# Optimization experiments

Hardware: AMD Instinct MI355X
Metric: run time of the kernel (lower is better)

## Reference

```python
import jax, jax.numpy as jnp
import numpy as np

N_NODES = 50000
N_EDGES = 800000
G_DIM = 128
H1 = 32
HEADS = 4
H2 = 64
ATT_SLOPE = 0.2   # PyG GATConv default negative_slope
LRELU_SLOPE = 0.01  # F.leaky_relu default
BN_EPS = 1e-5


def segment_softmax(logits, seg, num_segments):
    # numerically stable softmax over edges grouped by destination node
    m = jax.ops.segment_max(logits, seg, num_segments=num_segments)
    e = jnp.exp(logits - m[seg])
    s = jax.ops.segment_sum(e, seg, num_segments=num_segments)
    return e / (s[seg] + 1e-16)


def gat_layer(x, src, dst, W, a_src, a_dst, bias, concat):
    # PyG GATConv: x' = W x ; alpha_e = softmax_dst(leaky_relu(a_src.x_src + a_dst.x_dst))
    N = x.shape[0]
    H, C = a_src.shape
    xw = (x @ W).reshape(N, H, C)          # [N,H,C]
    al_s = jnp.sum(xw * a_src, axis=-1)    # [N,H]
    al_d = jnp.sum(xw * a_dst, axis=-1)    # [N,H]
    logits = jax.nn.leaky_relu(al_s[src] + al_d[dst], ATT_SLOPE)  # [E,H]
    alpha = segment_softmax(logits, dst, N)                        # [E,H]
    out = jax.ops.segment_sum(alpha[:, :, None] * xw[src], dst, num_segments=N)  # [N,H,C]
    out = out.reshape(N, H * C) if concat else out.mean(axis=1)
    return out + bias


def batchnorm_train(x, gamma, beta):
    mu = x.mean(axis=0)
    var = x.var(axis=0)  # biased, as torch BN uses for normalization
    return (x - mu) * jax.lax.rsqrt(var + BN_EPS) * gamma + beta


def setup_inputs() -> dict:
    key = jax.random.key(0)
    ks = jax.random.split(key, 12)
    node_features = jax.random.normal(ks[0], (N_NODES, G_DIM), dtype=jnp.float32)
    node_type = jax.random.randint(ks[1], (N_NODES,), 0, 3)
    edge_index = jax.random.randint(ks[2], (2, N_EDGES), 0, N_NODES)
    s1 = 1.0 / np.sqrt(G_DIM)
    s2 = 1.0 / np.sqrt(H1 * HEADS)
    return {
        "node_features": node_features,
        "node_type": node_type,
        "edge_index": edge_index,
        "W1": jax.random.normal(ks[3], (G_DIM, HEADS * H1), dtype=jnp.float32) * s1,
        "a_src1": jax.random.normal(ks[4], (HEADS, H1), dtype=jnp.float32) * s1,
        "a_dst1": jax.random.normal(ks[5], (HEADS, H1), dtype=jnp.float32) * s1,
        "b1": jnp.zeros((HEADS * H1,), dtype=jnp.float32),
        "g1": jnp.ones((HEADS * H1,), dtype=jnp.float32),
        "beta1": jnp.zeros((HEADS * H1,), dtype=jnp.float32),
        "W2": jax.random.normal(ks[6], (HEADS * H1, H2), dtype=jnp.float32) * s2,
        "a_src2": jax.random.normal(ks[7], (1, H2), dtype=jnp.float32) * s2,
        "a_dst2": jax.random.normal(ks[8], (1, H2), dtype=jnp.float32) * s2,
        "b2": jnp.zeros((H2,), dtype=jnp.float32),
        "g2": jnp.ones((H2,), dtype=jnp.float32),
        "beta2": jnp.zeros((H2,), dtype=jnp.float32),
    }


def reference(node_features, node_type, edge_index, W1, a_src1, a_dst1, b1, g1, beta1,
              W2, a_src2, a_dst2, b2, g2, beta2):
    N = node_features.shape[0]
    loop = jnp.arange(N)
    src = jnp.concatenate([edge_index[0], loop])  # add_self_loops=True (PyG default)
    dst = jnp.concatenate([edge_index[1], loop])
    x = gat_layer(node_features, src, dst, W1, a_src1, a_dst1, b1, concat=True)
    x = jax.nn.leaky_relu(batchnorm_train(x, g1, beta1), LRELU_SLOPE)
    x = gat_layer(x, src, dst, W2, a_src2, a_dst2, b2, concat=False)
    x = jax.nn.leaky_relu(batchnorm_train(x, g2, beta2), LRELU_SLOPE)
    return x
```

## Files before the change

kernel.cpp:

```cpp
#include <hip/hip_runtime.h>
#include <hip/hip_fp16.h>

#define NN 50000
#define NE 800000
#define ET 850000
#define GD 128
#define D1 128
#define NH 4
#define D2 64
#define NB_SCAN 196
#define NBP 1024
#define NXCD 8
#define NPX 6250
#define HSL 128
#define ESL 6250
#define NHB 1024
#define CAP 1024

typedef unsigned short u16;
typedef _Float16 half8_t __attribute__((ext_vector_type(8)));
typedef float    f32x4_t __attribute__((ext_vector_type(4)));

__device__ __forceinline__ float lrelu(float x, float s) { return x > 0.f ? x : s * x; }

__global__ void k_prepw(const float* __restrict__ W1, const float* __restrict__ W2,
                        __half* __restrict__ Wp1, __half* __restrict__ Wp2) {
    int idx = blockIdx.x * 256 + threadIdx.x;
    if (idx < 16384) {
        int i = idx & 7, l = (idx >> 3) & 63, nt = (idx >> 9) & 7, kk = idx >> 12;
        int k = kk * 32 + (l >> 4) * 8 + i, n = nt * 16 + (l & 15);
        Wp1[idx] = __float2half(W1[k * D1 + n]);
    } else if (idx < 24576) {
        int x2 = idx - 16384;
        int i = x2 & 7, l = (x2 >> 3) & 63, nt = (x2 >> 9) & 3, kk = x2 >> 11;
        int k = kk * 32 + (l >> 4) * 8 + i, n = nt * 16 + (l & 15);
        Wp2[x2] = __float2half(W2[k * D2 + n]);
    }
}

__global__ void k_histgemm1(const int* __restrict__ ei,
                            unsigned* __restrict__ ulist, u16* __restrict__ plist,
                            u16* __restrict__ partial, int* __restrict__ mcount,
                            const float* __restrict__ x, const half8_t* __restrict__ wp,
                            const float* __restrict__ as, const float* __restrict__ ad,
                            __half* __restrict__ xw, float* __restrict__ al_s,
                            float* __restrict__ al_d) {
    __shared__ unsigned lh[NPX / 2];
    __shared__ unsigned lk;
    if (blockIdx.x < NHB) {
        const int s = blockIdx.x & (NXCD - 1), j = blockIdx.x >> 3;
        const int lo = s * NPX;
        for (int i = threadIdx.x; i < NPX / 2; i += 256) lh[i] = 0u;
        if (threadIdx.x == 0) lk = 0u;
        __syncthreads();
        const int e0 = j * ESL;
        const size_t ub = (size_t)blockIdx.x * CAP;
        for (int e = e0 + threadIdx.x; e < e0 + ESL; e += 256) {
            int d = ei[NE + e];
            unsigned dl = (unsigned)(d - lo);
            if (dl < (unsigned)NPX) {
                unsigned old = atomicAdd(&lh[dl >> 1], (dl & 1) ? 0x10000u : 1u);
                unsigned p = (old >> ((dl & 1) * 16)) & 0xffffu;
                unsigned k = atomicAdd(&lk, 1u);
                if (k < CAP) {
                    ulist[ub + k] = (dl << 16) | (unsigned)ei[e];
                    plist[ub + k] = (u16)p;
                }
            }
        }
        __syncthreads();
        unsigned* pout = (unsigned*)(partial + (size_t)blockIdx.x * NPX);
        for (int i = threadIdx.x; i < NPX / 2; i += 256) pout[i] = lh[i];
        if (threadIdx.x == 0) mcount[blockIdx.x] = (int)lk;
        return;
    }
    const int strip = (blockIdx.x - NHB) * 4 + (threadIdx.x >> 6);
    if (strip >= NN / 16) return;
    const int l = threadIdx.x & 63;
    const int row0 = strip * 16;
    const int c = l & 15, g = l >> 4;
    const float* xrow = x + (size_t)(row0 + c) * GD;

    f32x4_t acc[8];
#pragma unroll
    for (int nt = 0; nt < 8; nt++) acc[nt] = (f32x4_t){0.f, 0.f, 0.f, 0.f};

#pragma unroll
    for (int kk = 0; kk < 4; kk++) {
        const int koff = kk * 32 + g * 8;
        f32x4_t a0 = *(const f32x4_t*)(xrow + koff);
        f32x4_t a1 = *(const f32x4_t*)(xrow + koff + 4);
        half8_t af;
#pragma unroll
        for (int i = 0; i < 4; i++) { af[i] = (_Float16)a0[i]; af[i + 4] = (_Float16)a1[i]; }
#pragma unroll
        for (int nt = 0; nt < 8; nt++) {
            half8_t bf = wp[(kk * 8 + nt) * 64 + l];
            acc[nt] = __builtin_amdgcn_mfma_f32_16x16x32_f16(af, bf, acc[nt], 0, 0, 0);
        }
    }

    float asv[8], adv[8];
#pragma unroll
    for (int nt = 0; nt < 8; nt++) { asv[nt] = as[nt * 16 + c]; adv[nt] = ad[nt * 16 + c]; }

#pragma unroll
    for (int r = 0; r < 4; r++) {
        const int row = row0 + g * 4 + r;
        __half* xwr = xw + (size_t)row * D1;
        float hs[4] = {0.f, 0.f, 0.f, 0.f}, hd[4] = {0.f, 0.f, 0.f, 0.f};
#pragma unroll
        for (int nt = 0; nt < 8; nt++) {
            float v = acc[nt][r];
            xwr[nt * 16 + c] = __float2half(v);
            hs[nt >> 1] += v * asv[nt];
            hd[nt >> 1] += v * adv[nt];
        }
#pragma unroll
        for (int m = 1; m <= 8; m <<= 1) {
#pragma unroll
            for (int h = 0; h < 4; h++) { hs[h] += __shfl_xor(hs[h], m); hd[h] += __shfl_xor(hd[h], m); }
        }
        if (c == 0) {
#pragma unroll
            for (int h = 0; h < 4; h++) { al_s[row * NH + h] = hs[h]; al_d[row * NH + h] = hd[h]; }
        }
    }
}

__global__ void k_nodeprefix(u16* __restrict__ partial, int* __restrict__ cnt) {
    int d = blockIdx.x * 256 + threadIdx.x;
    if (d >= NN) return;
    int s = d / NPX, dl = d - s * NPX;
    int run = 0;
    for (int j = 0; j < HSL; j++) {
        size_t idx = (size_t)(j * NXCD + s) * NPX + dl;
        int v = partial[idx];
        partial[idx] = (u16)run;
        run += v;
    }
    cnt[d] = run + 1;
}

__global__ void k_blocksum(const int* __restrict__ cnt, int* __restrict__ part) {
    __shared__ int r[256];
    int t = threadIdx.x, i = blockIdx.x * 256 + t;
    r[t] = (i < NN) ? cnt[i] : 0;
    __syncthreads();
    for (int s = 128; s >= 1; s >>= 1) {
        if (t < s) r[t] += r[t + s];
        __syncthreads();
    }
    if (t == 0) part[blockIdx.x] = r[0];
}

__global__ void k_scanfix(const int* __restrict__ cnt, const int* __restrict__ part,
                          int* __restrict__ row_ptr) {
    __shared__ int pp[256];
    __shared__ int r[256];
    int b = blockIdx.x, t = threadIdx.x, i = b * 256 + t;
    pp[t] = (t < NB_SCAN) ? part[t] : 0;
    int v = (i < NN) ? cnt[i] : 0;
    r[t] = v;
    __syncthreads();
    for (int off = 1; off < 256; off <<= 1) {
        int pv = (t >= off) ? pp[t - off] : 0;
        int rv = (t >= off) ? r[t - off] : 0;
        __syncthreads();
        pp[t] += pv; r[t] += rv;
        __syncthreads();
    }
    int pbase = b ? pp[b - 1] : 0;
    if (i < NN) row_ptr[i] = pbase + (t ? r[t - 1] : 0);
    if (i == NN - 1) row_ptr[NN] = pbase + r[t];
}

__global__ void k_fill_x(const int* __restrict__ row_ptr, const u16* __restrict__ P,
                         const unsigned* __restrict__ ulist, const u16* __restrict__ plist,
                         const int* __restrict__ mcount, u16* __restrict__ csr_src) {
    const int b = blockIdx.x;
    if (b < NHB) {
        const int s = b & (NXCD - 1);
        const int lo = s * NPX;
        const int m = min(mcount[b], CAP);
        const size_t ub = (size_t)b * CAP;
        const u16* Pb = P + (size_t)b * NPX;
        for (int k = threadIdx.x; k < m; k += 256) {
            unsigned u = ulist[ub + k];
            int dl = (int)(u >> 16);
            int base = row_ptr[lo + dl] + 1 + (int)Pb[dl] + (int)plist[ub + k];
            csr_src[base] = (u16)(u & 0xffffu);
        }
        return;
    }
    const int b2 = b - NHB;
    const int xcd = b2 & (NXCD - 1);
    const int off = (b2 >> 3) * 256 + threadIdx.x;
    if (off < NPX) {
        int d = xcd * NPX + off;
        csr_src[row_ptr[d]] = (u16)d;
    }
}

__global__ void k_gat1(const int* __restrict__ row_ptr, const u16* __restrict__ csr_src,
                       const float* __restrict__ als, const float* __restrict__ ald,
                       const __half2* __restrict__ xw, __half2* __restrict__ out) {
    const int b = blockIdx.x;
    const int d = (b & (NXCD - 1)) * NPX + (b >> 3);
    const int beg = row_ptr[d];
    const int deg = row_ptr[d + 1] - beg;
    const int lane = threadIdx.x;

    __shared__ int   s_src[64];
    __shared__ float s_al[64 * NH];

    const float4 adv = *(const float4*)(ald + d * NH);
    const int h = lane >> 4;

    float ax = 0.f, ay = 0.f, den = 0.f;
    for (int base = 0; base < deg; base += 64) {
        int cnt = min(64, deg - base);
        if (lane < cnt) {
            int s = csr_src[beg + base + lane];
            s_src[lane] = s;
            const float4 a = *(const float4*)(als + s * NH);
            s_al[lane * NH + 0] = __expf(lrelu(a.x + adv.x, 0.2f));
            s_al[lane * NH + 1] = __expf(lrelu(a.y + adv.y, 0.2f));
            s_al[lane * NH + 2] = __expf(lrelu(a.z + adv.z, 0.2f));
            s_al[lane * NH + 3] = __expf(lrelu(a.w + adv.w, 0.2f));
        }
        __syncthreads();
#pragma unroll 4
        for (int i = 0; i < cnt; i++) {
            float al = s_al[i * NH + h];
            float2 v = __half22float2(xw[(size_t)s_src[i] * 64 + lane]);
            den += al; ax += al * v.x; ay += al * v.y;
        }
        __syncthreads();
    }
    float inv = 1.f / (den + 1e-16f);
    __half2 hv;
    hv.x = __float2half(ax * inv);
    hv.y = __float2half(ay * inv);
    out[(size_t)d * 64 + lane] = hv;
}

__global__ void k_bnstats1h(const __half2* __restrict__ x, float* __restrict__ bp) {
    int t = threadIdx.x, bid = blockIdx.x;
    float s0 = 0.f, q0 = 0.f, s1 = 0.f, q1 = 0.f;
    for (int r = bid; r < NN; r += NBP) {
        float2 f = __half22float2(x[(size_t)r * 64 + t]);
        s0 += f.x; q0 += f.x * f.x;
        s1 += f.y; q1 += f.y * f.y;
    }
    bp[bid * D1 + 2 * t] = s0;
    bp[bid * D1 + 2 * t + 1] = s1;
    bp[NBP * D1 + bid * D1 + 2 * t] = q0;
    bp[NBP * D1 + bid * D1 + 2 * t + 1] = q1;
}

template <int D>
__global__ void k_bnstats(const float* __restrict__ x, float* __restrict__ bp) {
    int j = threadIdx.x, bid = blockIdx.x;
    float s = 0.f, q = 0.f;
    for (int r = bid; r < NN; r += NBP) {
        float v = x[(size_t)r * D + j];
        s += v; q += v * v;
    }
    bp[bid * D + j] = s;
    bp[NBP * D + bid * D + j] = q;
}

template <int D>
__global__ void k_bnreduce(const float* __restrict__ bp, const float* __restrict__ g,
                           const float* __restrict__ b, float* __restrict__ scale,
                           float* __restrict__ shift) {
    __shared__ float rs[256], rq[256];
    int j = blockIdx.x, t = threadIdx.x;
    float s = 0.f, q = 0.f;
    for (int i = t; i < NBP; i += 256) {
        s += bp[i * D + j];
        q += bp[NBP * D + i * D + j];
    }
    rs[t] = s; rq[t] = q;
    __syncthreads();
    for (int st = 128; st >= 1; st >>= 1) {
        if (t < st) { rs[t] += rs[t + st]; rq[t] += rq[t + st]; }
        __syncthreads();
    }
    if (t == 0) {
        float mu = rs[0] / (float)NN;
        float var = rq[0] / (float)NN - mu * mu;
        float sc = rsqrtf(var + 1e-5f) * g[j];
        scale[j] = sc;
        shift[j] = b[j] - mu * sc;
    }
}

__global__ void k_bnapply2(const float* __restrict__ x, const float* __restrict__ scale,
                           const float* __restrict__ shift, float* __restrict__ y) {
    int idx = blockIdx.x * blockDim.x + threadIdx.x;
    if (idx >= NN * D2 / 4) return;
    float4 v = ((const float4*)x)[idx];
    int c = (idx * 4) & (D2 - 1);
    v.x = lrelu(v.x * scale[c + 0] + shift[c + 0], 0.01f);
    v.y = lrelu(v.y * scale[c + 1] + shift[c + 1], 0.01f);
    v.z = lrelu(v.z * scale[c + 2] + shift[c + 2], 0.01f);
    v.w = lrelu(v.w * scale[c + 3] + shift[c + 3], 0.01f);
    ((float4*)y)[idx] = v;
}

__global__ void k_gemm2m(const __half* __restrict__ x, const float* __restrict__ scale,
                         const float* __restrict__ shift, const half8_t* __restrict__ wp,
                         const float* __restrict__ as, const float* __restrict__ ad,
                         __half* __restrict__ xw, float* __restrict__ al_s, float* __restrict__ al_d) {
    const int l = threadIdx.x;
    const int row0 = blockIdx.x * 16;
    const int c = l & 15, g = l >> 4;
    const __half* xrow = x + (size_t)(row0 + c) * D1;

    f32x4_t acc[4];
#pragma unroll
    for (int nt = 0; nt < 4; nt++) acc[nt] = (f32x4_t){0.f, 0.f, 0.f, 0.f};

#pragma unroll
    for (int kk = 0; kk < 4; kk++) {
        const int koff = kk * 32 + g * 8;
        half8_t a8 = *(const half8_t*)(xrow + koff);
        f32x4_t sc0 = *(const f32x4_t*)(scale + koff);
        f32x4_t sc1 = *(const f32x4_t*)(scale + koff + 4);
        f32x4_t sh0 = *(const f32x4_t*)(shift + koff);
        f32x4_t sh1 = *(const f32x4_t*)(shift + koff + 4);
        half8_t af;
#pragma unroll
        for (int i = 0; i < 4; i++) {
            af[i]     = (_Float16)lrelu((float)a8[i] * sc0[i] + sh0[i], 0.01f);
            af[i + 4] = (_Float16)lrelu((float)a8[i + 4] * sc1[i] + sh1[i], 0.01f);
        }
#pragma unroll
        for (int nt = 0; nt < 4; nt++) {
            half8_t bf = wp[(kk * 4 + nt) * 64 + l];
            acc[nt] = __builtin_amdgcn_mfma_f32_16x16x32_f16(af, bf, acc[nt], 0, 0, 0);
        }
    }

    float asv[4], adv[4];
#pragma unroll
    for (int nt = 0; nt < 4; nt++) { asv[nt] = as[nt * 16 + c]; adv[nt] = ad[nt * 16 + c]; }

#pragma unroll
    for (int r = 0; r < 4; r++) {
        const int row = row0 + g * 4 + r;
        __half* xwr = xw + (size_t)row * D2;
        float hs = 0.f, hd = 0.f;
#pragma unroll
        for (int nt = 0; nt < 4; nt++) {
            float v = acc[nt][r];
            xwr[nt * 16 + c] = __float2half(v);
            hs += v * asv[nt];
            hd += v * adv[nt];
        }
#pragma unroll
        for (int m = 1; m <= 8; m <<= 1) { hs += __shfl_xor(hs, m); hd += __shfl_xor(hd, m); }
        if (c == 0) { al_s[row] = hs; al_d[row] = hd; }
    }
}

__global__ void k_gat2(const int* __restrict__ row_ptr, const u16* __restrict__ csr_src,
                       const float* __restrict__ als, const float* __restrict__ ald,
                       const __half2* __restrict__ xw, float* __restrict__ out) {
    const int b = blockIdx.x;
    const int d = (b & (NXCD - 1)) * NPX + (b >> 3);
    const int beg = row_ptr[d];
    const int deg = row_ptr[d + 1] - beg;
    const int lane = threadIdx.x;
    const int sub = lane >> 5, l = lane & 31;

    const float add = ald[d];
    float ax = 0.f, ay = 0.f, den = 0.f;
    for (int base = 0; base < deg; base += 64) {
        int cnt = min(64, deg - base);
        int s = 0; float e = 0.f;
        if (lane < cnt) {
            s = csr_src[beg + base + lane];
            e = __expf(lrelu(als[s] + add, 0.2f));
        }
        int np = (cnt + 1) >> 1;
        for (int i = 0; i < np; i++) {
            int idx = 2 * i + sub;
            float al = __shfl(e, idx);
            int  si  = __shfl(s, idx);
            float2 v = __half22float2(xw[(size_t)si * 32 + l]);
            den += al; ax += al * v.x; ay += al * v.y;
        }
    }
    ax += __shfl_xor(ax, 32); ay += __shfl_xor(ay, 32); den += __shfl_xor(den, 32);
    if (lane < 32) {
        float inv = 1.f / (den + 1e-16f);
        *(float2*)(out + (size_t)d * D2 + 2 * l) = make_float2(ax * inv, ay * inv);
    }
}

extern "C" void kernel_launch(void* const* d_in, const int* in_sizes, int n_in,
                              void* d_out, int out_size, void* d_ws, size_t ws_size,
                              hipStream_t stream) {
    const float* x   = (const float*)d_in[0];
    const int*   ei  = (const int*)d_in[2];
    const float* W1  = (const float*)d_in[3];
    const float* as1 = (const float*)d_in[4];
    const float* ad1 = (const float*)d_in[5];
    const float* g1  = (const float*)d_in[7];
    const float* be1 = (const float*)d_in[8];
    const float* W2  = (const float*)d_in[9];
    const float* as2 = (const float*)d_in[10];
    const float* ad2 = (const float*)d_in[11];
    const float* g2  = (const float*)d_in[13];
    const float* be2 = (const float*)d_in[14];
    float* out = (float*)d_out;

    float* ws = (float*)d_ws;
    __half* xw1  = (__half*)ws;
    __half* xw2  = (__half*)ws;
    float* bp    = ws + 1600000;
    unsigned* ulist = (unsigned*)(ws + 3200000);
    u16*   plist  = (u16*)(ws + 4248576);
    int*   mcount = (int*)(ws + 4772864);
    int*   cnt    = (int*)(ws + 4773888);
    float* al_s2 = ws + 3200000;
    float* al_d2 = ws + 3250000;
    float* al_s1 = ws + 6400000;
    float* al_d1 = al_s1 + 200000;
    float* aggF  = al_d1 + 200000;
    __half* agg1 = (__half*)aggF;
    u16*   partial = (u16*)aggF;
    int*   row_ptr = (int*)(aggF + 3200000);
    int*   part    = row_ptr + 50001;
    float* st      = (float*)(part + 249);
    u16*   csr_src = (u16*)(st + 768);
    __half* Wp1    = (__half*)(csr_src + 850000);
    __half* Wp2    = Wp1 + 16384;

    k_prepw<<<96, 256, 0, stream>>>(W1, W2, Wp1, Wp2);
    k_histgemm1<<<NHB + (NN / 16 + 3) / 4, 256, 0, stream>>>(
        ei, ulist, plist, partial, mcount, x, (const half8_t*)Wp1, as1, ad1, xw1, al_s1, al_d1);
    k_nodeprefix<<<NB_SCAN, 256, 0, stream>>>(partial, cnt);
    k_blocksum<<<NB_SCAN, 256, 0, stream>>>(cnt, part);
    k_scanfix<<<NB_SCAN, 256, 0, stream>>>(cnt, part, row_ptr);
    k_fill_x<<<NHB + 200, 256, 0, stream>>>(row_ptr, partial, ulist, plist, mcount, csr_src);

    k_gat1<<<NN, 64, 0, stream>>>(row_ptr, csr_src, al_s1, al_d1, (const __half2*)xw1,
                                  (__half2*)agg1);
    k_bnstats1h<<<NBP, 64, 0, stream>>>((const __half2*)agg1, bp);
    k_bnreduce<D1><<<D1, 256, 0, stream>>>(bp, g1, be1, st, st + 128);

    k_gemm2m<<<NN / 16, 64, 0, stream>>>(agg1, st, st + 128, (const half8_t*)Wp2, as2, ad2,
                                         xw2, al_s2, al_d2);
    k_gat2<<<NN, 64, 0, stream>>>(row_ptr, csr_src, al_s2, al_d2, (const __half2*)xw2, out);
    k_bnstats<D2><<<NBP, D2, 0, stream>>>(out, bp);
    k_bnreduce<D2><<<D2, 256, 0, stream>>>(bp, g2, be2, st + 256, st + 320);
    k_bnapply2<<<(NN * D2 / 4 + 255) / 256, 256, 0, stream>>>(out, st + 256, st + 320, out);
}
```

Baseline: 182.2 us.

## Pack four destination nodes per block in GAT kernels and fuse prefix with blocksum

The two GAT aggregation kernels now handle four destination nodes per 256-thread block, one wavefront each, instead of one 64-thread block per node. This cuts block count and launch/scheduling overhead. k_gat1 also drops its shared-memory staging and __syncthreads, passing source indices and attention weights between lanes with shuffles. The per-node prefix kernel and the block-sum kernel are merged into one launch. The trade-off is five shuffles per edge in k_gat1 and some idle waves in the tail blocks.

After: 213.2 us. +17.0%, slower.

```diff
diff --git a/kernel.cpp b/kernel.cpp
--- a/kernel.cpp
+++ b/kernel.cpp
@@ -16,6 +16,7 @@
 #define ESL 6250
 #define NHB 1024
 #define CAP 1024
+#define NGB (NXCD * 1563)
 
 typedef unsigned short u16;
 typedef _Float16 half8_t __attribute__((ext_vector_type(8)));
@@ -128,27 +129,26 @@
     }
 }
 
-__global__ void k_nodeprefix(u16* __restrict__ partial, int* __restrict__ cnt) {
-    int d = blockIdx.x * 256 + threadIdx.x;
-    if (d >= NN) return;
-    int s = d / NPX, dl = d - s * NPX;
+__global__ void k_prefsum(u16* __restrict__ partial, int* __restrict__ cnt,
+                          int* __restrict__ part) {
+    __shared__ int r[256];
+    int t = threadIdx.x, d = blockIdx.x * 256 + t;
     int run = 0;
-    for (int j = 0; j < HSL; j++) {
-        size_t idx = (size_t)(j * NXCD + s) * NPX + dl;
-        int v = partial[idx];
-        partial[idx] = (u16)run;
-        run += v;
-    }
-    cnt[d] = run + 1;
-}
-
-__global__ void k_blocksum(const int* __restrict__ cnt, int* __restrict__ part) {
-    __shared__ int r[256];
-    int t = threadIdx.x, i = blockIdx.x * 256 + t;
-    r[t] = (i < NN) ? cnt[i] : 0;
+    if (d < NN) {
+        int s = d / NPX, dl = d - s * NPX;
+        for (int j = 0; j < HSL; j++) {
+            size_t idx = (size_t)(j * NXCD + s) * NPX + dl;
+            int v = partial[idx];
+            partial[idx] = (u16)run;
+            run += v;
+        }
+        run += 1;
+        cnt[d] = run;
+    }
+    r[t] = (d < NN) ? run : 0;
     __syncthreads();
-    for (int s = 128; s >= 1; s >>= 1) {
-        if (t < s) r[t] += r[t + s];
+    for (int s2 = 128; s2 >= 1; s2 >>= 1) {
+        if (t < s2) r[t] += r[t + s2];
         __syncthreads();
     }
     if (t == 0) part[blockIdx.x] = r[0];
@@ -205,38 +205,39 @@
 __global__ void k_gat1(const int* __restrict__ row_ptr, const u16* __restrict__ csr_src,
                        const float* __restrict__ als, const float* __restrict__ ald,
                        const __half2* __restrict__ xw, __half2* __restrict__ out) {
-    const int b = blockIdx.x;
-    const int d = (b & (NXCD - 1)) * NPX + (b >> 3);
+    const int bi = blockIdx.x;
+    const int s = bi & (NXCD - 1);
+    const int off = (bi >> 3) * 4 + (threadIdx.x >> 6);
+    if (off >= NPX) return;
+    const int d = s * NPX + off;
+    const int lane = threadIdx.x & 63;
     const int beg = row_ptr[d];
     const int deg = row_ptr[d + 1] - beg;
-    const int lane = threadIdx.x;
-
-    __shared__ int   s_src[64];
-    __shared__ float s_al[64 * NH];
+    const int h = lane >> 4;
 
     const float4 adv = *(const float4*)(ald + d * NH);
-    const int h = lane >> 4;
 
     float ax = 0.f, ay = 0.f, den = 0.f;
     for (int base = 0; base < deg; base += 64) {
         int cnt = min(64, deg - base);
+        int sv = 0;
+        float e0 = 0.f, e1 = 0.f, e2 = 0.f, e3 = 0.f;
         if (lane < cnt) {
-            int s = csr_src[beg + base + lane];
-            s_src[lane] = s;
-            const float4 a = *(const float4*)(als + s * NH);
-            s_al[lane * NH + 0] = __expf(lrelu(a.x + adv.x, 0.2f));
-            s_al[lane * NH + 1] = __expf(lrelu(a.y + adv.y, 0.2f));
-            s_al[lane * NH + 2] = __expf(lrelu(a.z + adv.z, 0.2f));
-            s_al[lane * NH + 3] = __expf(lrelu(a.w + adv.w, 0.2f));
-        }
-        __syncthreads();
-#pragma unroll 4
+            sv = csr_src[beg + base + lane];
+            const float4 a = *(const float4*)(als + sv * NH);
+            e0 = __expf(lrelu(a.x + adv.x, 0.2f));
+            e1 = __expf(lrelu(a.y + adv.y, 0.2f));
+            e2 = __expf(lrelu(a.z + adv.z, 0.2f));
+            e3 = __expf(lrelu(a.w + adv.w, 0.2f));
+        }
         for (int i = 0; i < cnt; i++) {
-            float al = s_al[i * NH + h];
-            float2 v = __half22float2(xw[(size_t)s_src[i] * 64 + lane]);
+            float a0 = __shfl(e0, i), a1 = __shfl(e1, i);
+            float a2 = __shfl(e2, i), a3 = __shfl(e3, i);
+            int   si = __shfl(sv, i);
+            float al = (h == 0) ? a0 : (h == 1) ? a1 : (h == 2) ? a2 : a3;
+            float2 v = __half22float2(xw[(size_t)si * 64 + lane]);
             den += al; ax += al * v.x; ay += al * v.y;
         }
-        __syncthreads();
     }
     float inv = 1.f / (den + 1e-16f);
     __half2 hv;
@@ -369,27 +370,30 @@
 __global__ void k_gat2(const int* __restrict__ row_ptr, const u16* __restrict__ csr_src,
                        const float* __restrict__ als, const float* __restrict__ ald,
                        const __half2* __restrict__ xw, float* __restrict__ out) {
-    const int b = blockIdx.x;
-    const int d = (b & (NXCD - 1)) * NPX + (b >> 3);
+    const int bi = blockIdx.x;
+    const int s = bi & (NXCD - 1);
+    const int off = (bi >> 3) * 4 + (threadIdx.x >> 6);
+    if (off >= NPX) return;
+    const int d = s * NPX + off;
+    const int lane = threadIdx.x & 63;
     const int beg = row_ptr[d];
     const int deg = row_ptr[d + 1] - beg;
-    const int lane = threadIdx.x;
     const int sub = lane >> 5, l = lane & 31;
 
     const float add = ald[d];
     float ax = 0.f, ay = 0.f, den = 0.f;
     for (int base = 0; base < deg; base += 64) {
         int cnt = min(64, deg - base);
-        int s = 0; float e = 0.f;
+        int sv = 0; float e = 0.f;
         if (lane < cnt) {
-            s = csr_src[beg + base + lane];
-            e = __expf(lrelu(als[s] + add, 0.2f));
+            sv = csr_src[beg + base + lane];
+            e = __expf(lrelu(als[sv] + add, 0.2f));
         }
         int np = (cnt + 1) >> 1;
         for (int i = 0; i < np; i++) {
             int idx = 2 * i + sub;
             float al = __shfl(e, idx);
-            int  si  = __shfl(s, idx);
+            int  si  = __shfl(sv, idx);
             float2 v = __half22float2(xw[(size_t)si * 32 + l]);
             den += al; ax += al * v.x; ay += al * v.y;
         }
@@ -443,19 +447,18 @@
     k_prepw<<<96, 256, 0, stream>>>(W1, W2, Wp1, Wp2);
     k_histgemm1<<<NHB + (NN / 16 + 3) / 4, 256, 0, stream>>>(
         ei, ulist, plist, partial, mcount, x, (const half8_t*)Wp1, as1, ad1, xw1, al_s1, al_d1);
-    k_nodeprefix<<<NB_SCAN, 256, 0, stream>>>(partial, cnt);
-    k_blocksum<<<NB_SCAN, 256, 0, stream>>>(cnt, part);
+    k_prefsum<<<NB_SCAN, 256, 0, stream>>>(partial, cnt, part);
     k_scanfix<<<NB_SCAN, 256, 0, stream>>>(cnt, part, row_ptr);
     k_fill_x<<<NHB + 200, 256, 0, stream>>>(row_ptr, partial, ulist, plist, mcount, csr_src);
 
-    k_gat1<<<NN, 64, 0, stream>>>(row_ptr, csr_src, al_s1, al_d1, (const __half2*)xw1,
-                                  (__half2*)agg1);
+    k_gat1<<<NGB, 256, 0, stream>>>(row_ptr, csr_src, al_s1, al_d1, (const __half2*)xw1,
+                                    (__half2*)agg1);
     k_bnstats1h<<<NBP, 64, 0, stream>>>((const __half2*)agg1, bp);
     k_bnreduce<D1><<<D1, 256, 0, stream>>>(bp, g1, be1, st, st + 128);
 
     k_gemm2m<<<NN / 16, 64, 0, stream>>>(agg1, st, st + 128, (const half8_t*)Wp2, as2, ad2,
                                          xw2, al_s2, al_d2);
-    k_gat2<<<NN, 64, 0, stream>>>(row_ptr, csr_src, al_s2, al_d2, (const __half2*)xw2, out);
+    k_gat2<<<NGB, 256, 0, stream>>>(row_ptr, csr_src, al_s2, al_d2, (const __half2*)xw2, out);
     k_bnstats<D2><<<NBP, D2, 0, stream>>>(out, bp);
     k_bnreduce<D2><<<D2, 256, 0, stream>>>(bp, g2, be2, st + 256, st + 320);
     k_bnapply2<<<(NN * D2 / 4 + 255) / 256, 256, 0, stream>>>(out, st + 256, st + 320, out);
```
